# Kernel optimization log

Measured on AMD Instinct MI355X. Metric: run time of the kernel, lower is better.

The kernel has to match this reference:

```python
import jax, jax.numpy as jnp
import numpy as np

N = 200_000      # n_reflns
NIMG = 500       # n_images
DMETA = 24       # metadata features
WIDTH = 32       # mlp_width
HID = 64         # hidden_units = 2*width (FeedForward default)
DEPTH = 20       # mlp_depth
NPOST = 2        # Normal posterior: (loc, scale)
EPS = 1e-12
KLW = 0.01       # scaling_kl_weight


def setup_inputs() -> dict:
    key = jax.random.key(0)
    ks = jax.random.split(key, 10)
    metadata = jax.random.normal(ks[0], (N, DMETA), jnp.float32)
    iobs = jax.random.normal(ks[1], (N, 1), jnp.float32)
    sigiobs = jax.random.uniform(ks[2], (N, 1), jnp.float32)
    image_ids = jnp.sort(jax.random.randint(ks[3], (N,), 0, NIMG)).astype(jnp.int32)
    n_reflns_per_image = jnp.bincount(image_ids, length=NIMG).astype(jnp.int32)
    d_img = DMETA + 2  # concat(metadata, iobs, sigiobs)
    w_img_in = jax.random.normal(ks[4], (d_img, WIDTH), jnp.float32) / np.float32(np.sqrt(d_img))
    b_img_in = jnp.zeros((WIDTH,), jnp.float32)
    w_scale_in = jax.random.normal(ks[5], (DMETA, WIDTH), jnp.float32) / np.float32(np.sqrt(DMETA))
    b_scale_in = jnp.zeros((WIDTH,), jnp.float32)
    # shared residual FeedForward stack (share_weights=True): x + W2 @ relu(W1 @ x)
    mlp_w1 = jax.random.normal(ks[6], (DEPTH, WIDTH, HID), jnp.float32) / np.float32(np.sqrt(WIDTH))
    mlp_b1 = jnp.zeros((DEPTH, HID), jnp.float32)
    mlp_w2 = jax.random.normal(ks[7], (DEPTH, HID, WIDTH), jnp.float32) * np.float32(0.1 / np.sqrt(HID))
    mlp_b2 = jnp.zeros((DEPTH, WIDTH), jnp.float32)
    w_out = jax.random.normal(ks[8], (WIDTH, NPOST), jnp.float32) / np.float32(np.sqrt(WIDTH))
    b_out = jnp.zeros((NPOST,), jnp.float32)
    return {
        'metadata': metadata, 'iobs': iobs, 'sigiobs': sigiobs,
        'w_img_in': w_img_in, 'b_img_in': b_img_in,
        'w_scale_in': w_scale_in, 'b_scale_in': b_scale_in,
        'mlp_w1': mlp_w1, 'mlp_b1': mlp_b1, 'mlp_w2': mlp_w2, 'mlp_b2': mlp_b2,
        'w_out': w_out, 'b_out': b_out,
        'image_ids_in_this_batch': image_ids,
        'n_reflns_per_image': n_reflns_per_image,
        'mc_samples': 32,
    }


def _mlp(h, w1, b1, w2, b2):
    # depth residual FF blocks, weights stacked along leading DEPTH axis
    def block(h, ws):
        wa, ba, wb, bb = ws
        h = h + (jax.nn.relu(h @ wa + ba) @ wb + bb)
        return h, None
    h, _ = jax.lax.scan(block, h, (w1, b1, w2, b2))
    return h


def reference(metadata, iobs, sigiobs,
              w_img_in, b_img_in, w_scale_in, b_scale_in,
              mlp_w1, mlp_b1, mlp_w2, mlp_b2, w_out, b_out,
              image_ids_in_this_batch, n_reflns_per_image, mc_samples):
    image = jnp.concatenate([metadata, iobs, sigiobs], axis=-1)   # (N, DMETA+2)
    h = image @ w_img_in + b_img_in                               # (N, W)
    h = _mlp(h, mlp_w1, mlp_b1, mlp_w2, mlp_b2)
    nimg = n_reflns_per_image.shape[0]
    sums = jax.ops.segment_sum(h, image_ids_in_this_batch, num_segments=nimg)
    counts = jnp.maximum(n_reflns_per_image, 1).astype(h.dtype)[:, None]
    pooled = sums / counts                                        # (NIMG, W) image-average pool
    s = metadata @ w_scale_in + b_scale_in + pooled[image_ids_in_this_batch]
    s = _mlp(s, mlp_w1, mlp_b1, mlp_w2, mlp_b2)                   # shared weights
    params = s @ w_out + b_out                                    # (N, 2)
    loc = params[:, 0]
    scale = jax.nn.softplus(params[:, 1]) + EPS
    # rsample from Normal(loc, scale), mc_samples draws
    noise = jax.random.normal(jax.random.key(42), (mc_samples, loc.shape[0]), loc.dtype)
    z = loc + scale * noise                                       # (S, N)
    # MC KL estimate: mean_s[log q(z) - log p(z)], p = Laplace(0, 1)
    log_q = -0.5 * jnp.square(noise) - jnp.log(scale) - np.float32(0.5 * np.log(2.0 * np.pi))
    log_p = -jnp.abs(z) - np.float32(np.log(2.0))
    kl_div = KLW * jnp.mean(log_q - log_p, axis=0)                # (N,)
    return z.T, kl_div
```

## Files before the change

kernel.cpp:

```cpp
#include <hip/hip_runtime.h>
#include <stdint.h>

#define N_ROWS 200000
#define NIMG   500
#define DMETA  24
#define WIDTH  32
#define HID    64
#define DEPTH  20
#define MC     32
#define NSTR   18

typedef __attribute__((ext_vector_type(8))) short bf16x8;
typedef __attribute__((ext_vector_type(4))) float f32x4;

#define MFMA(a, b, acc) __builtin_amdgcn_mfma_f32_16x16x32_bf16((a), (b), (acc), 0, 0, 0)

#define OFF_W1H  64000
#define OFF_W1L  145920
#define OFF_W2H  227840
#define OFF_W2L  309760
#define OFF_WIH  391680
#define OFF_WIL  393728
#define OFF_WSH  395776
#define OFF_WSL  397824

__device__ __forceinline__ uint32_t rotl32(uint32_t x, int r) {
    return (x << r) | (x >> (32 - r));
}

__device__ __forceinline__ uint32_t tf_bits(uint32_t j) {
    const uint32_t ks1 = 42u, ks2 = 0x1BD11BDAu ^ 42u;
    uint32_t x0 = 0u, x1 = j + ks1;
#define R4(a,b,c,d) \
    x0 += x1; x1 = rotl32(x1,(a)); x1 ^= x0; \
    x0 += x1; x1 = rotl32(x1,(b)); x1 ^= x0; \
    x0 += x1; x1 = rotl32(x1,(c)); x1 ^= x0; \
    x0 += x1; x1 = rotl32(x1,(d)); x1 ^= x0;
    R4(13,15,26,6)  x0 += ks1; x1 += ks2 + 1u;
    R4(17,29,16,24) x0 += ks2; x1 += 0u + 2u;
    R4(13,15,26,6)                x1 += ks1 + 3u;
    R4(17,29,16,24) x0 += ks1; x1 += ks2 + 4u;
    R4(13,15,26,6)  x0 += ks2; x1 += 0u + 5u;
#undef R4
    return x0 ^ x1;
}

__device__ __forceinline__ float bits_to_normal(uint32_t b) {
    float f = __uint_as_float((b >> 9) | 0x3f800000u) - 1.0f;
    const float lo = -0.99999994f;
    float u = fmaxf(lo, f * 2.0f + lo);
    return 1.41421356f * erfinvf(u);
}

__device__ __forceinline__ void split1(float x, short& hi, short& lo) {
    uint32_t b = __float_as_uint(x);
    uint32_t a = b + 0x8000u;
    hi = (short)(a >> 16);
    float r = x - __uint_as_float(a & 0xFFFF0000u);
    lo = (short)(__float_as_uint(r) >> 16);
}

__device__ __forceinline__ void split8p(const float* x, bf16x8& hi, bf16x8& lo) {
    uint32_t hu[4], lu[4];
#pragma unroll
    for (int p = 0; p < 4; ++p) {
        uint32_t b0 = __float_as_uint(x[2 * p]);
        uint32_t b1 = __float_as_uint(x[2 * p + 1]);
        uint32_t a0 = b0 + 0x8000u, a1 = b1 + 0x8000u;
        hu[p] = __builtin_amdgcn_perm(a1, a0, 0x07060302u);
        float r0 = x[2 * p] - __uint_as_float(a0 & 0xFFFF0000u);
        float r1 = x[2 * p + 1] - __uint_as_float(a1 & 0xFFFF0000u);
        lu[p] = __builtin_amdgcn_perm(__float_as_uint(r1), __float_as_uint(r0), 0x07060302u);
    }
    __builtin_memcpy(&hi, hu, 16);
    __builtin_memcpy(&lo, lu, 16);
}

__device__ __forceinline__ void mlp20_x2(
    float* hC0, float* hC1, float* smw0, float* smw1,
    const short* __restrict__ w1fh, const short* __restrict__ w1fl,
    const short* __restrict__ w2fh, const short* __restrict__ w2fl,
    const float* __restrict__ b1, const float* __restrict__ b2,
    int lane, int q, int c) {
    float2* sm20 = (float2*)smw0;
    float2* sm21 = (float2*)smw1;
#pragma unroll 1
    for (int l = 0; l < DEPTH; ++l) {
#pragma unroll
        for (int t = 0; t < 2; ++t) {
            int bi = (16 * t + c) * 9 + 2 * q;
            sm20[bi]     = make_float2(hC0[t * 4 + 0], hC0[t * 4 + 1]);
            sm20[bi + 1] = make_float2(hC0[t * 4 + 2], hC0[t * 4 + 3]);
            sm21[bi]     = make_float2(hC1[t * 4 + 0], hC1[t * 4 + 1]);
            sm21[bi + 1] = make_float2(hC1[t * 4 + 2], hC1[t * 4 + 3]);
        }
        float a0[8], a1[8];
#pragma unroll
        for (int j = 0; j < 8; ++j) a0[j] = smw0[(q * 8 + j) * NSTR + c];
#pragma unroll
        for (int j = 0; j < 8; ++j) a1[j] = smw1[(q * 8 + j) * NSTR + c];
        bf16x8 ah0, al0, ah1, al1;
        split8p(a0, ah0, al0);
        split8p(a1, ah1, al1);
        float C1v0[16], C1v1[16];
#pragma unroll
        for (int t = 0; t < 4; ++t) {
            const int fi = (((l * 4 + t) << 9) + (lane << 3));
            bf16x8 bh = *(const bf16x8*)(w1fh + fi);
            bf16x8 bl = *(const bf16x8*)(w1fl + fi);
            float bb = b1[l * 64 + 16 * t + c];
            f32x4 acc = {0.f, 0.f, 0.f, 0.f};
            acc = MFMA(ah0, bh, acc); acc = MFMA(ah0, bl, acc); acc = MFMA(al0, bh, acc);
            f32x4 acd = {0.f, 0.f, 0.f, 0.f};
            acd = MFMA(ah1, bh, acd); acd = MFMA(ah1, bl, acd); acd = MFMA(al1, bh, acd);
#pragma unroll
            for (int r = 0; r < 4; ++r) {
                C1v0[t * 4 + r] = fmaxf(acc[r] + bb, 0.0f);
                C1v1[t * 4 + r] = fmaxf(acd[r] + bb, 0.0f);
            }
        }
#pragma unroll
        for (int t = 0; t < 4; ++t) {
            int bi = (16 * t + c) * 9 + 2 * q;
            sm20[bi]     = make_float2(C1v0[t * 4 + 0], C1v0[t * 4 + 1]);
            sm20[bi + 1] = make_float2(C1v0[t * 4 + 2], C1v0[t * 4 + 3]);
            sm21[bi]     = make_float2(C1v1[t * 4 + 0], C1v1[t * 4 + 1]);
            sm21[bi + 1] = make_float2(C1v1[t * 4 + 2], C1v1[t * 4 + 3]);
        }
        f32x4 acc0[2], acc1[2];
#pragma unroll
        for (int t2 = 0; t2 < 2; ++t2)
#pragma unroll
            for (int r = 0; r < 4; ++r) {
                acc0[t2][r] = hC0[t2 * 4 + r];
                acc1[t2][r] = hC1[t2 * 4 + r];
            }
#pragma unroll
        for (int kf = 0; kf < 2; ++kf) {
            float e0[8], e1[8];
#pragma unroll
            for (int j = 0; j < 8; ++j) e0[j] = smw0[(kf * 32 + q * 8 + j) * NSTR + c];
#pragma unroll
            for (int j = 0; j < 8; ++j) e1[j] = smw1[(kf * 32 + q * 8 + j) * NSTR + c];
            bf16x8 xh0, xl0, xh1, xl1;
            split8p(e0, xh0, xl0);
            split8p(e1, xh1, xl1);
#pragma unroll
            for (int t2 = 0; t2 < 2; ++t2) {
                const int fi = ((((l * 2 + kf) * 2 + t2) << 9) + (lane << 3));
                bf16x8 bh = *(const bf16x8*)(w2fh + fi);
                bf16x8 bl = *(const bf16x8*)(w2fl + fi);
                acc0[t2] = MFMA(xh0, bh, acc0[t2]);
                acc0[t2] = MFMA(xh0, bl, acc0[t2]);
                acc0[t2] = MFMA(xl0, bh, acc0[t2]);
                acc1[t2] = MFMA(xh1, bh, acc1[t2]);
                acc1[t2] = MFMA(xh1, bl, acc1[t2]);
                acc1[t2] = MFMA(xl1, bh, acc1[t2]);
            }
        }
#pragma unroll
        for (int t2 = 0; t2 < 2; ++t2) {
            float bb = b2[l * 32 + 16 * t2 + c];
#pragma unroll
            for (int r = 0; r < 4; ++r) {
                hC0[t2 * 4 + r] = acc0[t2][r] + bb;
                hC1[t2 * 4 + r] = acc1[t2][r] + bb;
            }
        }
    }
}

__device__ __forceinline__ void input_proj(
    const bf16x8& ah, const bf16x8& al, const short* __restrict__ wfh,
    const short* __restrict__ wfl, const float* __restrict__ bias,
    float* hC, int lane, int c) {
#pragma unroll
    for (int t = 0; t < 2; ++t) {
        bf16x8 bh = *(const bf16x8*)(wfh + ((t << 9) + (lane << 3)));
        bf16x8 bl = *(const bf16x8*)(wfl + ((t << 9) + (lane << 3)));
        f32x4 acc = {0.f, 0.f, 0.f, 0.f};
        acc = MFMA(ah, bh, acc); acc = MFMA(ah, bl, acc); acc = MFMA(al, bh, acc);
        float bb = bias[16 * t + c];
#pragma unroll
        for (int r = 0; r < 4; ++r) hC[t * 4 + r] = acc[r] + bb;
    }
}

__global__ __launch_bounds__(256) void prep_kernel(
    const float* __restrict__ w1, const float* __restrict__ w2,
    const float* __restrict__ wimg, const float* __restrict__ wsc,
    char* __restrict__ wsb) {
    int t = blockIdx.x * 256 + threadIdx.x;
    float* sums = (float*)wsb;
    if (t < 16000) { sums[t] = 0.0f; return; }
    t -= 16000;
    if (t < 40960) {
        int l = t >> 11, r = t & 2047, tt = r >> 9, r2 = r & 511;
        int lane = r2 >> 3, j = r2 & 7;
        int k = (lane >> 4) * 8 + j, n = 16 * tt + (lane & 15);
        short h, lo;
        split1(w1[l * 2048 + k * 64 + n], h, lo);
        ((short*)(wsb + OFF_W1H))[t] = h;
        ((short*)(wsb + OFF_W1L))[t] = lo;
        return;
    }
    t -= 40960;
    if (t < 40960) {
        int l = t >> 11, r = t & 2047, kf = r >> 10, r2 = r & 1023;
        int t2 = r2 >> 9, r3 = r2 & 511, lane = r3 >> 3, j = r3 & 7;
        int k = kf * 32 + (lane >> 4) * 8 + j, n = 16 * t2 + (lane & 15);
        short h, lo;
        split1(w2[l * 2048 + k * 32 + n], h, lo);
        ((short*)(wsb + OFF_W2H))[t] = h;
        ((short*)(wsb + OFF_W2L))[t] = lo;
        return;
    }
    t -= 40960;
    if (t < 1024) {
        int tt = t >> 9, r = t & 511, lane = r >> 3, j = r & 7;
        int k = (lane >> 4) * 8 + j, n = 16 * tt + (lane & 15);
        float v = (k < 26) ? wimg[k * 32 + n] : 0.0f;
        short h, lo;
        split1(v, h, lo);
        ((short*)(wsb + OFF_WIH))[t] = h;
        ((short*)(wsb + OFF_WIL))[t] = lo;
        return;
    }
    t -= 1024;
    if (t < 1024) {
        int tt = t >> 9, r = t & 511, lane = r >> 3, j = r & 7;
        int k = (lane >> 4) * 8 + j, n = 16 * tt + (lane & 15);
        float v = (k < 24) ? wsc[k * 32 + n] : 0.0f;
        short h, lo;
        split1(v, h, lo);
        ((short*)(wsb + OFF_WSH))[t] = h;
        ((short*)(wsb + OFF_WSL))[t] = lo;
        return;
    }
}

__device__ __forceinline__ void load_xfrag(
    const float* __restrict__ md, const float* __restrict__ iobs,
    const float* __restrict__ sig, int base, int q, int c,
    bf16x8& ah, bf16x8& al) {
    float xa[8];
    if (q < 3) {
        const f32x4* rp = (const f32x4*)(md + (size_t)(base + c) * DMETA + q * 8);
        f32x4 v0 = rp[0], v1 = rp[1];
#pragma unroll
        for (int j = 0; j < 4; ++j) { xa[j] = v0[j]; xa[4 + j] = v1[j]; }
    } else {
        xa[0] = iobs ? iobs[base + c] : 0.0f;
        xa[1] = sig ? sig[base + c] : 0.0f;
#pragma unroll
        for (int j = 2; j < 8; ++j) xa[j] = 0.0f;
    }
    split8p(xa, ah, al);
}

__global__ __launch_bounds__(128, 4) void pass_a(
    const float* __restrict__ md, const float* __restrict__ iobs,
    const float* __restrict__ sig, const float* __restrict__ bimg,
    const char* __restrict__ wsb, const float* __restrict__ b1,
    const float* __restrict__ b2, const int* __restrict__ ids,
    float* __restrict__ sums) {
    __shared__ float smat[2][2][64 * NSTR];
    int lane = threadIdx.x & 63, w = threadIdx.x >> 6;
    int q = lane >> 4, c = lane & 15;
    int i0 = (blockIdx.x * 2 + w) * 32;
    float* smw0 = &smat[w][0][0];
    float* smw1 = &smat[w][1][0];

    bf16x8 ah0, al0, ah1, al1;
    load_xfrag(md, iobs, sig, i0, q, c, ah0, al0);
    load_xfrag(md, iobs, sig, i0 + 16, q, c, ah1, al1);

    float hC0[8], hC1[8];
    input_proj(ah0, al0, (const short*)(wsb + OFF_WIH), (const short*)(wsb + OFF_WIL),
               bimg, hC0, lane, c);
    input_proj(ah1, al1, (const short*)(wsb + OFF_WIH), (const short*)(wsb + OFF_WIL),
               bimg, hC1, lane, c);

    mlp20_x2(hC0, hC1, smw0, smw1,
             (const short*)(wsb + OFF_W1H), (const short*)(wsb + OFF_W1L),
             (const short*)(wsb + OFF_W2H), (const short*)(wsb + OFF_W2L),
             b1, b2, lane, q, c);

#pragma unroll
    for (int tile = 0; tile < 2; ++tile) {
        const float* hC = tile ? hC1 : hC0;
        int tb = i0 + tile * 16;
        bool uni = (ids[tb] == ids[tb + 15]);
        if (uni) {
            int id = ids[tb];
#pragma unroll
            for (int t = 0; t < 2; ++t) {
                float s = (hC[t * 4 + 0] + hC[t * 4 + 1]) + (hC[t * 4 + 2] + hC[t * 4 + 3]);
                s += __shfl_xor(s, 16, 64);
                s += __shfl_xor(s, 32, 64);
                if (q == 0) atomicAdd(&sums[id * 32 + 16 * t + c], s);
            }
        } else {
            int idv[4];
#pragma unroll
            for (int r = 0; r < 4; ++r) idv[r] = ids[tb + q * 4 + r];
#pragma unroll
            for (int t = 0; t < 2; ++t)
#pragma unroll
                for (int r = 0; r < 4; ++r)
                    atomicAdd(&sums[idv[r] * 32 + 16 * t + c], hC[t * 4 + r]);
        }
    }
}

__global__ __launch_bounds__(256) void normalize_kernel(float* __restrict__ sums,
                                                        const int* __restrict__ cnts) {
    int t = blockIdx.x * 256 + threadIdx.x;
    if (t < NIMG * WIDTH) {
        int img = t >> 5;
        float cc = (float)max(cnts[img], 1);
        sums[t] = sums[t] / cc;
    }
}

__global__ __launch_bounds__(128, 4) void pass_b(
    const float* __restrict__ md, const float* __restrict__ bsc,
    const char* __restrict__ wsb, const float* __restrict__ b1,
    const float* __restrict__ b2, const float* __restrict__ wout,
    const float* __restrict__ bout, const int* __restrict__ ids,
    const float* __restrict__ pooled, float* __restrict__ out) {
    __shared__ float smat[2][2][64 * NSTR];
    __shared__ float sls[2][64];
    int lane = threadIdx.x & 63, w = threadIdx.x >> 6;
    int q = lane >> 4, c = lane & 15;
    int i0 = (blockIdx.x * 2 + w) * 32;
    float* smw0 = &smat[w][0][0];
    float* smw1 = &smat[w][1][0];

    bf16x8 ah0, al0, ah1, al1;
    load_xfrag(md, nullptr, nullptr, i0, q, c, ah0, al0);
    load_xfrag(md, nullptr, nullptr, i0 + 16, q, c, ah1, al1);

    float hC0[8], hC1[8];
    input_proj(ah0, al0, (const short*)(wsb + OFF_WSH), (const short*)(wsb + OFF_WSL),
               bsc, hC0, lane, c);
    input_proj(ah1, al1, (const short*)(wsb + OFF_WSH), (const short*)(wsb + OFF_WSL),
               bsc, hC1, lane, c);
#pragma unroll
    for (int tile = 0; tile < 2; ++tile) {
        float* hC = tile ? hC1 : hC0;
        int tb = i0 + tile * 16;
        int idv[4];
#pragma unroll
        for (int r = 0; r < 4; ++r) idv[r] = ids[tb + q * 4 + r];
#pragma unroll
        for (int t = 0; t < 2; ++t)
#pragma unroll
            for (int r = 0; r < 4; ++r)
                hC[t * 4 + r] += pooled[idv[r] * 32 + 16 * t + c];
    }

    mlp20_x2(hC0, hC1, smw0, smw1,
             (const short*)(wsb + OFF_W1H), (const short*)(wsb + OFF_W1L),
             (const short*)(wsb + OFF_W2H), (const short*)(wsb + OFF_W2L),
             b1, b2, lane, q, c);

    float wo0[2], wo1[2];
#pragma unroll
    for (int t = 0; t < 2; ++t) {
        float2 wv = ((const float2*)wout)[16 * t + c];
        wo0[t] = wv.x; wo1[t] = wv.y;
    }
#pragma unroll
    for (int tile = 0; tile < 2; ++tile) {
        const float* hC = tile ? hC1 : hC0;
        float p0r[4], p1r[4];
#pragma unroll
        for (int r = 0; r < 4; ++r) {
            p0r[r] = hC[r] * wo0[0] + hC[4 + r] * wo0[1];
            p1r[r] = hC[r] * wo1[0] + hC[4 + r] * wo1[1];
        }
#pragma unroll
        for (int m = 1; m < 16; m <<= 1) {
#pragma unroll
            for (int r = 0; r < 4; ++r) {
                p0r[r] += __shfl_xor(p0r[r], m, 64);
                p1r[r] += __shfl_xor(p1r[r], m, 64);
            }
        }
        if (c == 0) {
#pragma unroll
            for (int r = 0; r < 4; ++r) {
                float loc = p0r[r] + bout[0];
                float pb = p1r[r] + bout[1];
                float scale = fmaxf(pb, 0.0f) + log1pf(expf(-fabsf(pb))) + 1e-12f;
                sls[w][tile * 16 + q * 4 + r] = loc;
                sls[w][32 + tile * 16 + q * 4 + r] = scale;
            }
        }
    }

    int ro = lane & 31, half = lane >> 5;
    int row = i0 + ro;
    float L = sls[w][ro];
    float S = sls[w][32 + ro];
    float lsg = logf(S);
    float kp = 0.0f;
    float* zrow = out + (size_t)row * MC + half * 16;
#pragma unroll 4
    for (int s4 = 0; s4 < 4; ++s4) {
        f32x4 zv;
#pragma unroll
        for (int jj = 0; jj < 4; ++jj) {
            int t = half * 16 + s4 * 4 + jj;
            uint32_t j = (uint32_t)(t * N_ROWS) + (uint32_t)row;
            float n = bits_to_normal(tf_bits(j));
            float z = fmaf(S, n, L);
            zv[jj] = z;
            kp += fmaf(-0.5f, n * n, fabsf(z));
        }
        *(f32x4*)(zrow + s4 * 4) = zv;
    }
    kp += __shfl_xor(kp, 32, 64);
    if (half == 0) {
        out[(size_t)N_ROWS * MC + row] =
            0.01f * (kp * (1.0f / 32.0f) - lsg - 0.91893853320467274f + 0.69314718055994531f);
    }
}

extern "C" void kernel_launch(void* const* d_in, const int* in_sizes, int n_in,
                              void* d_out, int out_size, void* d_ws, size_t ws_size,
                              hipStream_t stream) {
    const float* md   = (const float*)d_in[0];
    const float* iobs = (const float*)d_in[1];
    const float* sig  = (const float*)d_in[2];
    const float* wimg = (const float*)d_in[3];
    const float* bimg = (const float*)d_in[4];
    const float* wsc  = (const float*)d_in[5];
    const float* bsc  = (const float*)d_in[6];
    const float* w1   = (const float*)d_in[7];
    const float* b1   = (const float*)d_in[8];
    const float* w2   = (const float*)d_in[9];
    const float* b2   = (const float*)d_in[10];
    const float* wout = (const float*)d_in[11];
    const float* bout = (const float*)d_in[12];
    const int* ids    = (const int*)d_in[13];
    const int* cnts   = (const int*)d_in[14];
    float* out = (float*)d_out;
    char* wsb = (char*)d_ws;
    float* sums = (float*)wsb;

    const int nblk = N_ROWS / 64;
    prep_kernel<<<391, 256, 0, stream>>>(w1, w2, wimg, wsc, wsb);
    pass_a<<<nblk, 128, 0, stream>>>(md, iobs, sig, bimg, wsb, b1, b2, ids, sums);
    normalize_kernel<<<(NIMG * WIDTH + 255) / 256, 256, 0, stream>>>(sums, cnts);
    pass_b<<<nblk, 128, 0, stream>>>(md, bsc, wsb, b1, b2, wout, bout, ids, sums, out);
}
```

Baseline: 394.4 us.

## Interleave per-layer weights and biases, transpose LDS tile for vector reads, fold bias into MFMA

Repacks the split bf16 hi/lo weights and both bias vectors into one contiguous block per layer, so the MLP loop walks a single base pointer with fixed offsets and reads biases as vector loads. It also changes the LDS staging tile to a row-major layout with stride 68, so the MFMA operand gather becomes two 16-byte LDS reads instead of eight scalar reads. Biases are now used as the initial MFMA accumulator rather than added afterwards. The scalar LDS stores on the write side may hit more bank conflicts.

```diff
diff --git a/kernel.cpp b/kernel.cpp
--- a/kernel.cpp
+++ b/kernel.cpp
@@ -8,21 +8,21 @@
 #define HID    64
 #define DEPTH  20
 #define MC     32
-#define NSTR   18
+
+#define LSTRIDE_F 68
+#define TILE_F    (16 * LSTRIDE_F)
+
+#define WB    64000
+#define LSTR  16768
+#define OFF_WIH (WB + DEPTH * LSTR)
+#define OFF_WIL (OFF_WIH + 2048)
+#define OFF_WSH (OFF_WIH + 4096)
+#define OFF_WSL (OFF_WIH + 6144)
 
 typedef __attribute__((ext_vector_type(8))) short bf16x8;
 typedef __attribute__((ext_vector_type(4))) float f32x4;
 
 #define MFMA(a, b, acc) __builtin_amdgcn_mfma_f32_16x16x32_bf16((a), (b), (acc), 0, 0, 0)
-
-#define OFF_W1H  64000
-#define OFF_W1L  145920
-#define OFF_W2H  227840
-#define OFF_W2L  309760
-#define OFF_WIH  391680
-#define OFF_WIL  393728
-#define OFF_WSH  395776
-#define OFF_WSL  397824
 
 __device__ __forceinline__ uint32_t rotl32(uint32_t x, int r) {
     return (x << r) | (x >> (32 - r));
@@ -77,79 +77,94 @@
 }
 
 __device__ __forceinline__ void mlp20_x2(
-    float* hC0, float* hC1, float* smw0, float* smw1,
-    const short* __restrict__ w1fh, const short* __restrict__ w1fl,
-    const short* __restrict__ w2fh, const short* __restrict__ w2fl,
-    const float* __restrict__ b1, const float* __restrict__ b2,
+    float* hC0, float* hC1, float* smw, const char* __restrict__ wsb,
     int lane, int q, int c) {
-    float2* sm20 = (float2*)smw0;
-    float2* sm21 = (float2*)smw1;
+    const int ldsR = c * LSTRIDE_F + q * 8;
+    const int ldsW = q * 4 * LSTRIDE_F + c;
+    uint32_t offA  = (uint32_t)(WB + (lane << 4));
+    uint32_t offB  = offA + 4096u;
+    uint32_t offC  = offA + 8192u;
+    uint32_t offD  = offA + 12288u;
+    uint32_t offB1 = (uint32_t)(WB + 16384 + (c << 4));
+    uint32_t offB2 = (uint32_t)(WB + 16640 + (c << 3));
 #pragma unroll 1
     for (int l = 0; l < DEPTH; ++l) {
-#pragma unroll
-        for (int t = 0; t < 2; ++t) {
-            int bi = (16 * t + c) * 9 + 2 * q;
-            sm20[bi]     = make_float2(hC0[t * 4 + 0], hC0[t * 4 + 1]);
-            sm20[bi + 1] = make_float2(hC0[t * 4 + 2], hC0[t * 4 + 3]);
-            sm21[bi]     = make_float2(hC1[t * 4 + 0], hC1[t * 4 + 1]);
-            sm21[bi + 1] = make_float2(hC1[t * 4 + 2], hC1[t * 4 + 3]);
-        }
+        f32x4 b1v = *(const f32x4*)(wsb + offB1);
+        float2 b2v = *(const float2*)(wsb + offB2);
+#pragma unroll
+        for (int t = 0; t < 2; ++t)
+#pragma unroll
+            for (int r = 0; r < 4; ++r) {
+                smw[ldsW + r * LSTRIDE_F + t * 16] = hC0[t * 4 + r];
+                smw[TILE_F + ldsW + r * LSTRIDE_F + t * 16] = hC1[t * 4 + r];
+            }
+        f32x4 v0 = *(const f32x4*)(smw + ldsR);
+        f32x4 v1 = *(const f32x4*)(smw + ldsR + 4);
+        f32x4 u0 = *(const f32x4*)(smw + TILE_F + ldsR);
+        f32x4 u1 = *(const f32x4*)(smw + TILE_F + ldsR + 4);
         float a0[8], a1[8];
 #pragma unroll
-        for (int j = 0; j < 8; ++j) a0[j] = smw0[(q * 8 + j) * NSTR + c];
-#pragma unroll
-        for (int j = 0; j < 8; ++j) a1[j] = smw1[(q * 8 + j) * NSTR + c];
+        for (int j = 0; j < 4; ++j) {
+            a0[j] = v0[j]; a0[4 + j] = v1[j];
+            a1[j] = u0[j]; a1[4 + j] = u1[j];
+        }
         bf16x8 ah0, al0, ah1, al1;
         split8p(a0, ah0, al0);
         split8p(a1, ah1, al1);
         float C1v0[16], C1v1[16];
 #pragma unroll
         for (int t = 0; t < 4; ++t) {
-            const int fi = (((l * 4 + t) << 9) + (lane << 3));
-            bf16x8 bh = *(const bf16x8*)(w1fh + fi);
-            bf16x8 bl = *(const bf16x8*)(w1fl + fi);
-            float bb = b1[l * 64 + 16 * t + c];
-            f32x4 acc = {0.f, 0.f, 0.f, 0.f};
+            uint32_t o = (t < 2 ? offA : offB) + (uint32_t)((t & 1) << 11);
+            bf16x8 bh = *(const bf16x8*)(wsb + o);
+            bf16x8 bl = *(const bf16x8*)(wsb + o + 1024);
+            float bb = b1v[t];
+            f32x4 acc = {bb, bb, bb, bb};
             acc = MFMA(ah0, bh, acc); acc = MFMA(ah0, bl, acc); acc = MFMA(al0, bh, acc);
-            f32x4 acd = {0.f, 0.f, 0.f, 0.f};
+            f32x4 acd = {bb, bb, bb, bb};
             acd = MFMA(ah1, bh, acd); acd = MFMA(ah1, bl, acd); acd = MFMA(al1, bh, acd);
 #pragma unroll
             for (int r = 0; r < 4; ++r) {
-                C1v0[t * 4 + r] = fmaxf(acc[r] + bb, 0.0f);
-                C1v1[t * 4 + r] = fmaxf(acd[r] + bb, 0.0f);
-            }
-        }
-#pragma unroll
-        for (int t = 0; t < 4; ++t) {
-            int bi = (16 * t + c) * 9 + 2 * q;
-            sm20[bi]     = make_float2(C1v0[t * 4 + 0], C1v0[t * 4 + 1]);
-            sm20[bi + 1] = make_float2(C1v0[t * 4 + 2], C1v0[t * 4 + 3]);
-            sm21[bi]     = make_float2(C1v1[t * 4 + 0], C1v1[t * 4 + 1]);
-            sm21[bi + 1] = make_float2(C1v1[t * 4 + 2], C1v1[t * 4 + 3]);
-        }
+                C1v0[t * 4 + r] = fmaxf(acc[r], 0.0f);
+                C1v1[t * 4 + r] = fmaxf(acd[r], 0.0f);
+            }
+        }
+#pragma unroll
+        for (int t = 0; t < 4; ++t)
+#pragma unroll
+            for (int r = 0; r < 4; ++r) {
+                smw[ldsW + r * LSTRIDE_F + t * 16] = C1v0[t * 4 + r];
+                smw[TILE_F + ldsW + r * LSTRIDE_F + t * 16] = C1v1[t * 4 + r];
+            }
         f32x4 acc0[2], acc1[2];
 #pragma unroll
-        for (int t2 = 0; t2 < 2; ++t2)
-#pragma unroll
-            for (int r = 0; r < 4; ++r) {
-                acc0[t2][r] = hC0[t2 * 4 + r];
-                acc1[t2][r] = hC1[t2 * 4 + r];
-            }
+        for (int t2 = 0; t2 < 2; ++t2) {
+            float bb = t2 ? b2v.y : b2v.x;
+#pragma unroll
+            for (int r = 0; r < 4; ++r) {
+                acc0[t2][r] = hC0[t2 * 4 + r] + bb;
+                acc1[t2][r] = hC1[t2 * 4 + r] + bb;
+            }
+        }
 #pragma unroll
         for (int kf = 0; kf < 2; ++kf) {
+            f32x4 e0a = *(const f32x4*)(smw + ldsR + kf * 32);
+            f32x4 e0b = *(const f32x4*)(smw + ldsR + kf * 32 + 4);
+            f32x4 e1a = *(const f32x4*)(smw + TILE_F + ldsR + kf * 32);
+            f32x4 e1b = *(const f32x4*)(smw + TILE_F + ldsR + kf * 32 + 4);
             float e0[8], e1[8];
 #pragma unroll
-            for (int j = 0; j < 8; ++j) e0[j] = smw0[(kf * 32 + q * 8 + j) * NSTR + c];
-#pragma unroll
-            for (int j = 0; j < 8; ++j) e1[j] = smw1[(kf * 32 + q * 8 + j) * NSTR + c];
+            for (int j = 0; j < 4; ++j) {
+                e0[j] = e0a[j]; e0[4 + j] = e0b[j];
+                e1[j] = e1a[j]; e1[4 + j] = e1b[j];
+            }
             bf16x8 xh0, xl0, xh1, xl1;
             split8p(e0, xh0, xl0);
             split8p(e1, xh1, xl1);
 #pragma unroll
             for (int t2 = 0; t2 < 2; ++t2) {
-                const int fi = ((((l * 2 + kf) * 2 + t2) << 9) + (lane << 3));
-                bf16x8 bh = *(const bf16x8*)(w2fh + fi);
-                bf16x8 bl = *(const bf16x8*)(w2fl + fi);
+                uint32_t o = (kf ? offD : offC) + (uint32_t)(t2 << 11);
+                bf16x8 bh = *(const bf16x8*)(wsb + o);
+                bf16x8 bl = *(const bf16x8*)(wsb + o + 1024);
                 acc0[t2] = MFMA(xh0, bh, acc0[t2]);
                 acc0[t2] = MFMA(xh0, bl, acc0[t2]);
                 acc0[t2] = MFMA(xl0, bh, acc0[t2]);
@@ -159,14 +174,14 @@
             }
         }
 #pragma unroll
-        for (int t2 = 0; t2 < 2; ++t2) {
-            float bb = b2[l * 32 + 16 * t2 + c];
-#pragma unroll
-            for (int r = 0; r < 4; ++r) {
-                hC0[t2 * 4 + r] = acc0[t2][r] + bb;
-                hC1[t2 * 4 + r] = acc1[t2][r] + bb;
-            }
-        }
+        for (int t2 = 0; t2 < 2; ++t2)
+#pragma unroll
+            for (int r = 0; r < 4; ++r) {
+                hC0[t2 * 4 + r] = acc0[t2][r];
+                hC1[t2 * 4 + r] = acc1[t2][r];
+            }
+        offA += LSTR; offB += LSTR; offC += LSTR; offD += LSTR;
+        offB1 += LSTR; offB2 += LSTR;
     }
 }
 
@@ -178,17 +193,18 @@
     for (int t = 0; t < 2; ++t) {
         bf16x8 bh = *(const bf16x8*)(wfh + ((t << 9) + (lane << 3)));
         bf16x8 bl = *(const bf16x8*)(wfl + ((t << 9) + (lane << 3)));
-        f32x4 acc = {0.f, 0.f, 0.f, 0.f};
+        float bb = bias[16 * t + c];
+        f32x4 acc = {bb, bb, bb, bb};
         acc = MFMA(ah, bh, acc); acc = MFMA(ah, bl, acc); acc = MFMA(al, bh, acc);
-        float bb = bias[16 * t + c];
-#pragma unroll
-        for (int r = 0; r < 4; ++r) hC[t * 4 + r] = acc[r] + bb;
+#pragma unroll
+        for (int r = 0; r < 4; ++r) hC[t * 4 + r] = acc[r];
     }
 }
 
 __global__ __launch_bounds__(256) void prep_kernel(
     const float* __restrict__ w1, const float* __restrict__ w2,
     const float* __restrict__ wimg, const float* __restrict__ wsc,
+    const float* __restrict__ b1, const float* __restrict__ b2,
     char* __restrict__ wsb) {
     int t = blockIdx.x * 256 + threadIdx.x;
     float* sums = (float*)wsb;
@@ -200,8 +216,9 @@
         int k = (lane >> 4) * 8 + j, n = 16 * tt + (lane & 15);
         short h, lo;
         split1(w1[l * 2048 + k * 64 + n], h, lo);
-        ((short*)(wsb + OFF_W1H))[t] = h;
-        ((short*)(wsb + OFF_W1L))[t] = lo;
+        char* base = wsb + WB + l * LSTR + tt * 2048 + 2 * r2;
+        *(short*)(base) = h;
+        *(short*)(base + 1024) = lo;
         return;
     }
     t -= 40960;
@@ -211,8 +228,9 @@
         int k = kf * 32 + (lane >> 4) * 8 + j, n = 16 * t2 + (lane & 15);
         short h, lo;
         split1(w2[l * 2048 + k * 32 + n], h, lo);
-        ((short*)(wsb + OFF_W2H))[t] = h;
-        ((short*)(wsb + OFF_W2L))[t] = lo;
+        char* base = wsb + WB + l * LSTR + 8192 + (kf * 2 + t2) * 2048 + 2 * r3;
+        *(short*)(base) = h;
+        *(short*)(base + 1024) = lo;
         return;
     }
     t -= 40960;
@@ -237,6 +255,20 @@
         ((short*)(wsb + OFF_WSL))[t] = lo;
         return;
     }
+    t -= 1024;
+    if (t < 1280) {
+        int l = t >> 6, r = t & 63;
+        int c = r >> 2, tt = r & 3;
+        *(float*)(wsb + WB + l * LSTR + 16384 + 4 * r) = b1[l * 64 + tt * 16 + c];
+        return;
+    }
+    t -= 1280;
+    if (t < 640) {
+        int l = t >> 5, r = t & 31;
+        int c = r >> 1, t2 = r & 1;
+        *(float*)(wsb + WB + l * LSTR + 16640 + 4 * r) = b2[l * 32 + t2 * 16 + c];
+        return;
+    }
 }
 
 __device__ __forceinline__ void load_xfrag(
@@ -261,15 +293,13 @@
 __global__ __launch_bounds__(128, 4) void pass_a(
     const float* __restrict__ md, const float* __restrict__ iobs,
     const float* __restrict__ sig, const float* __restrict__ bimg,
-    const char* __restrict__ wsb, const float* __restrict__ b1,
-    const float* __restrict__ b2, const int* __restrict__ ids,
+    const char* __restrict__ wsb, const int* __restrict__ ids,
     float* __restrict__ sums) {
-    __shared__ float smat[2][2][64 * NSTR];
+    __shared__ __attribute__((aligned(16))) float smat[2][2 * TILE_F];
     int lane = threadIdx.x & 63, w = threadIdx.x >> 6;
     int q = lane >> 4, c = lane & 15;
     int i0 = (blockIdx.x * 2 + w) * 32;
-    float* smw0 = &smat[w][0][0];
-    float* smw1 = &smat[w][1][0];
+    float* smw = &smat[w][0];
 
     bf16x8 ah0, al0, ah1, al1;
     load_xfrag(md, iobs, sig, i0, q, c, ah0, al0);
@@ -281,10 +311,7 @@
     input_proj(ah1, al1, (const short*)(wsb + OFF_WIH), (const short*)(wsb + OFF_WIL),
                bimg, hC1, lane, c);
 
-    mlp20_x2(hC0, hC1, smw0, smw1,
-             (const short*)(wsb + OFF_W1H), (const short*)(wsb + OFF_W1L),
-             (const short*)(wsb + OFF_W2H), (const short*)(wsb + OFF_W2L),
-             b1, b2, lane, q, c);
+    mlp20_x2(hC0, hC1, smw, wsb, lane, q, c);
 
 #pragma unroll
     for (int tile = 0; tile < 2; ++tile) {
@@ -325,17 +352,15 @@
 
 __global__ __launch_bounds__(128, 4) void pass_b(
     const float* __restrict__ md, const float* __restrict__ bsc,
-    const char* __restrict__ wsb, const float* __restrict__ b1,
-    const float* __restrict__ b2, const float* __restrict__ wout,
+    const char* __restrict__ wsb, const float* __restrict__ wout,
     const float* __restrict__ bout, const int* __restrict__ ids,
     const float* __restrict__ pooled, float* __restrict__ out) {
-    __shared__ float smat[2][2][64 * NSTR];
+    __shared__ __attribute__((aligned(16))) float smat[2][2 * TILE_F];
     __shared__ float sls[2][64];
     int lane = threadIdx.x & 63, w = threadIdx.x >> 6;
     int q = lane >> 4, c = lane & 15;
     int i0 = (blockIdx.x * 2 + w) * 32;
-    float* smw0 = &smat[w][0][0];
-    float* smw1 = &smat[w][1][0];
+    float* smw = &smat[w][0];
 
     bf16x8 ah0, al0, ah1, al1;
     load_xfrag(md, nullptr, nullptr, i0, q, c, ah0, al0);
@@ -360,10 +385,7 @@
                 hC[t * 4 + r] += pooled[idv[r] * 32 + 16 * t + c];
     }
 
-    mlp20_x2(hC0, hC1, smw0, smw1,
-             (const short*)(wsb + OFF_W1H), (const short*)(wsb + OFF_W1L),
-             (const short*)(wsb + OFF_W2H), (const short*)(wsb + OFF_W2L),
-             b1, b2, lane, q, c);
+    mlp20_x2(hC0, hC1, smw, wsb, lane, q, c);
 
     float wo0[2], wo1[2];
 #pragma unroll
@@ -451,8 +473,8 @@
     float* sums = (float*)wsb;
 
     const int nblk = N_ROWS / 64;
-    prep_kernel<<<391, 256, 0, stream>>>(w1, w2, wimg, wsc, wsb);
-    pass_a<<<nblk, 128, 0, stream>>>(md, iobs, sig, bimg, wsb, b1, b2, ids, sums);
+    prep_kernel<<<398, 256, 0, stream>>>(w1, w2, wimg, wsc, b1, b2, wsb);
+    pass_a<<<nblk, 128, 0, stream>>>(md, iobs, sig, bimg, wsb, ids, sums);
     normalize_kernel<<<(NIMG * WIDTH + 255) / 256, 256, 0, stream>>>(sums, cnts);
-    pass_b<<<nblk, 128, 0, stream>>>(md, bsc, wsb, b1, b2, wout, bout, ids, sums, out);
-}
+    pass_b<<<nblk, 128, 0, stream>>>(md, bsc, wsb, wout, bout, ids, sums, out);
+}
```

Result: faster. 385.7 us (-2.2%).
